# Performance work log

Hardware: AMD Instinct MI355X
Metric: run time of the kernel (lower is better)

## Reference

```python
import jax, jax.numpy as jnp
import numpy as np

N_SEQ, N_TOK, C_M, C, C_Z = 512, 384, 64, 32, 128


def setup_inputs() -> dict:
    key = jax.random.key(0)
    k1, k2, k3, k4 = jax.random.split(key, 4)
    scale = 1.0 / np.sqrt(C_M)
    return {
        "msa_feat": jax.random.normal(k1, (N_SEQ, N_TOK, C_M), dtype=jnp.float32),
        "msa_mask": jnp.ones((N_SEQ, N_TOK), dtype=jnp.float32),
        "gamma": jnp.ones((C_M,), dtype=jnp.float32),
        "beta": jnp.zeros((C_M,), dtype=jnp.float32),
        "Wa": jax.random.normal(k2, (C_M, C), dtype=jnp.float32) * scale,
        "Wb": jax.random.normal(k3, (C_M, C), dtype=jnp.float32) * scale,
        "Wout": jax.random.normal(k4, (C * C, C_Z), dtype=jnp.float32) * (1.0 / C),
        "bout": jnp.zeros((C_Z,), dtype=jnp.float32),
    }


def reference(msa_feat, msa_mask, gamma, beta, Wa, Wb, Wout, bout):
    # LayerNorm over c_m (eps matches torch default 1e-5)
    mu = jnp.mean(msa_feat, axis=-1, keepdims=True)
    var = jnp.mean(jnp.square(msa_feat - mu), axis=-1, keepdims=True)
    m = (msa_feat - mu) * jax.lax.rsqrt(var + 1e-5) * gamma + beta

    mask = msa_mask[..., None]                       # [s, i, 1]
    a = (m @ Wa) * mask                              # [s, i, c]
    b = (m @ Wb) * mask                              # [s, j, c]

    # Outer product contracted over MSA rows s: [i, j, c, c]
    ab = jnp.einsum('sic,sjd->ijcd', a, b)
    n_tok = a.shape[-2]
    ab = ab.reshape(n_tok, n_tok, C * C)             # [i, j, c*c]

    z = ab @ Wout + bout                             # [i, j, c_z]
    norm = jnp.einsum('si,sj->ij', msa_mask, msa_mask)
    return z / (norm[..., None] + 0.001)
```

## Files before the change

### kernel.cpp

```cpp
#include <hip/hip_runtime.h>
#include <cstdint>
#include <cstddef>

#define NS 512
#define NT 384
#define CZ 128

typedef __bf16 bf16x8 __attribute__((ext_vector_type(8)));
typedef __bf16 bf16x4 __attribute__((ext_vector_type(4)));
typedef float floatx16 __attribute__((ext_vector_type(16)));
typedef float floatx4 __attribute__((ext_vector_type(4)));


__global__ __launch_bounds__(256) void prep_wout(const float* __restrict__ Wout,
                                                 __bf16* __restrict__ WT) {
  const int idx = blockIdx.x * 256 + threadIdx.x;
  const int e = idx >> 10, kk = idx & 1023;
  const int round = kk >> 9, rem = kk & 511, d = rem >> 4, cp = rem & 15;
  const int c = round * 16 + cp;
  WT[idx] = (__bf16)Wout[(size_t)(c * 32 + d) * CZ + e];
}

__global__ __launch_bounds__(256) void prep_norm(const float* __restrict__ mask,
                                                 float* __restrict__ rnorm) {
  __shared__ float mi[512];
  const int i = blockIdx.x, t = threadIdx.x;
  mi[t]       = mask[(size_t)t * NT + i];
  mi[t + 256] = mask[(size_t)(t + 256) * NT + i];
  __syncthreads();
  for (int j = t; j < NT; j += 256) {
    float acc = 0.f;
#pragma unroll 4
    for (int s = 0; s < NS; ++s) acc += mi[s] * mask[(size_t)s * NT + j];
    rnorm[(size_t)i * NT + j] = 1.0f / (acc + 0.001f);
  }
}

__global__ __launch_bounds__(64) void ln_proj(const float* __restrict__ feat,
                                              const float* __restrict__ mask,
                                              const float* __restrict__ gamma,
                                              const float* __restrict__ beta,
                                              const float* __restrict__ Wa,
                                              const float* __restrict__ Wb,
                                              __bf16* __restrict__ Abf,
                                              __bf16* __restrict__ Bbf) {
  __shared__ __align__(16) __bf16 T[32 * 72];
  const int bid = blockIdx.x;
  const int i = bid >> 3;
  const int s0 = (bid & 7) << 6;
  const int lane = threadIdx.x;
  const int l31 = lane & 31, lh = lane >> 5;

  const float* frow = feat + ((size_t)(s0 + lane) * NT + i) * 64;
  float x[64];
#pragma unroll
  for (int q = 0; q < 16; ++q) {
    const float4 v = *(const float4*)(frow + q * 4);
    x[q * 4 + 0] = v.x; x[q * 4 + 1] = v.y;
    x[q * 4 + 2] = v.z; x[q * 4 + 3] = v.w;
  }

  float mu = 0.f;
#pragma unroll
  for (int k = 0; k < 64; ++k) mu += x[k];
  mu *= (1.0f / 64.0f);
  float var = 0.f;
#pragma unroll
  for (int k = 0; k < 64; ++k) { const float d = x[k] - mu; var += d * d; }
  var *= (1.0f / 64.0f);
  const float rstd = rsqrtf(var + 1e-5f);
#pragma unroll
  for (int k = 0; k < 64; ++k)
    x[k] = (x[k] - mu) * rstd * gamma[k] + beta[k];

  const float mv = mask[(size_t)(s0 + lane) * NT + i];

  float acc[32];
#pragma unroll
  for (int c = 0; c < 32; ++c) acc[c] = 0.f;
#pragma unroll 8
  for (int k = 0; k < 64; ++k) {
    const float mk = x[k];
#pragma unroll
    for (int c = 0; c < 32; ++c) acc[c] = fmaf(mk, Wa[k * 32 + c], acc[c]);
  }
#pragma unroll
  for (int c = 0; c < 32; ++c) T[c * 72 + lane] = (__bf16)(acc[c] * mv);
  __syncthreads();
  {
    __bf16* dst = Abf + (size_t)(i >> 2) * 65536 + (size_t)(s0 >> 3) * 1024 +
                  (size_t)((i & 3) * 32) * 8;
#pragma unroll
    for (int q = 0; q < 4; ++q) {
      const bf16x8 v = *(const bf16x8*)(T + l31 * 72 + (q * 2 + lh) * 8);
      *(bf16x8*)(dst + (size_t)(q * 2 + lh) * 1024 + l31 * 8) = v;
    }
  }
  __syncthreads();

#pragma unroll
  for (int c = 0; c < 32; ++c) acc[c] = 0.f;
#pragma unroll 8
  for (int k = 0; k < 64; ++k) {
    const float mk = x[k];
#pragma unroll
    for (int c = 0; c < 32; ++c) acc[c] = fmaf(mk, Wb[k * 32 + c], acc[c]);
  }
#pragma unroll
  for (int c = 0; c < 32; ++c) T[c * 72 + lane] = (__bf16)(acc[c] * mv);
  __syncthreads();
  {
    __bf16* dst = Bbf + (size_t)(i >> 3) * 131072 + (size_t)(s0 >> 3) * 2048 +
                  (size_t)((i & 7) * 32) * 8;
#pragma unroll
    for (int q = 0; q < 4; ++q) {
      const bf16x8 v = *(const bf16x8*)(T + l31 * 72 + (q * 2 + lh) * 8);
      *(bf16x8*)(dst + (size_t)(q * 2 + lh) * 2048 + l31 * 8) = v;
    }
  }
}

__global__ __launch_bounds__(512, 4) void opm_gemm(const __bf16* __restrict__ A,
                                                   const __bf16* __restrict__ B,
                                                   const __bf16* __restrict__ WT,
                                                   const float* __restrict__ bout,
                                                   const float* __restrict__ rnorm,
                                                   float* __restrict__ out) {
  __shared__ __align__(16) __bf16 smem[24576];

  const int tid = threadIdx.x, lane = tid & 63, wid = tid >> 6;
  const int wm = wid & 1, wn = wid >> 1;
  const int l31 = lane & 31, lh = lane >> 5;
  const int l15 = lane & 15, lq = lane >> 4;
  const int bm = blockIdx.x % 96, bn = blockIdx.x / 96;

  const __bf16* Apan = A + (size_t)bm * 65536;
  const __bf16* Bpan = B + (size_t)bn * 131072;

  floatx16 acc[2][2];
#pragma unroll
  for (int fm = 0; fm < 2; ++fm)
#pragma unroll
    for (int fn = 0; fn < 2; ++fn)
#pragma unroll
      for (int q = 0; q < 16; ++q) acc[fm][fn][q] = 0.f;

#define STAGE(kt, OFF)                                                          \
  {                                                                             \
    __bf16* dst = smem + (OFF);                                                 \
    __builtin_amdgcn_global_load_lds(                                           \
        (const __attribute__((address_space(1))) void*)(Apan +                  \
            (size_t)(kt) * 4096 + wid * 512 + lane * 8),                        \
        (__attribute__((address_space(3))) void*)(dst + wid * 512), 16, 0, 0);  \
    _Pragma("unroll")                                                           \
    for (int q = 0; q < 2; ++q) {                                               \
      const int g = q * 8 + wid;                                                \
      __builtin_amdgcn_global_load_lds(                                         \
          (const __attribute__((address_space(1))) void*)(Bpan +                \
              (size_t)(kt) * 8192 + g * 512 + lane * 8),                        \
          (__attribute__((address_space(3))) void*)(dst + 4096 + g * 512),      \
          16, 0, 0);                                                            \
    }                                                                           \
  }

  STAGE(0, 0);
  int buf = 0;
  for (int kt = 0; kt < 16; ++kt) {
    __syncthreads();
    if (kt < 15) STAGE(kt + 1, (buf ^ 1) * 12288);
    const __bf16* As = smem + buf * 12288;
    const __bf16* Bs = As + 4096;
    __builtin_amdgcn_s_setprio(1);
#pragma unroll
    for (int ks = 0; ks < 2; ++ks) {
      const int ck = ks * 2 + lh;
      bf16x8 af[2], bfv[2];
#pragma unroll
      for (int fm = 0; fm < 2; ++fm)
        af[fm] = *(const bf16x8*)(As + ck * 1024 + (wm * 64 + fm * 32 + l31) * 8);
#pragma unroll
      for (int fn = 0; fn < 2; ++fn)
        bfv[fn] = *(const bf16x8*)(Bs + ck * 2048 + (wn * 64 + fn * 32 + l31) * 8);
#pragma unroll
      for (int fm = 0; fm < 2; ++fm)
#pragma unroll
        for (int fn = 0; fn < 2; ++fn)
          acc[fm][fn] = __builtin_amdgcn_mfma_f32_32x32x16_bf16(af[fm], bfv[fn],
                                                                acc[fm][fn], 0, 0, 0);
    }
    __builtin_amdgcn_s_setprio(0);
    buf ^= 1;
  }
#undef STAGE

  floatx4 zf[2];
#pragma unroll
  for (int ps = 0; ps < 2; ++ps)
#pragma unroll
    for (int q = 0; q < 4; ++q) zf[ps][q] = 0.f;
  const int e0 = wid * 16;

#pragma unroll
  for (int round = 0; round < 2; ++round) {
    __syncthreads();
#pragma unroll
    for (int fm = 0; fm < 2; ++fm)
#pragma unroll
      for (int fn = 0; fn < 2; ++fn) {
        const int p = (wm * 2 + fm) * 8 + wn * 2 + fn;
        __bf16* base = smem + p * 648 + l31 * 20 + lh * 4;
#pragma unroll
        for (int qp = 0; qp < 2; ++qp) {
          bf16x4 v;
#pragma unroll
          for (int j = 0; j < 4; ++j)
            v[j] = (__bf16)acc[fm][fn][round * 8 + qp * 4 + j];
          *(bf16x4*)(base + qp * 8) = v;
        }
      }
    __syncthreads();
    const int pAddr = (lq >> 1) * 20 + (lq & 1) * 8;
    const __bf16* p0 = smem + l15 * 648 + pAddr;
    const __bf16* p1 = p0 + 16 * 648;
    const __bf16* w0 = WT + (size_t)(e0 + l15) * 1024 + round * 512 + lq * 8;
#pragma unroll 4
    for (int ks = 0; ks < 16; ++ks) {
      const bf16x8 pa0 = *(const bf16x8*)(p0 + ks * 40);
      const bf16x8 pa1 = *(const bf16x8*)(p1 + ks * 40);
      const bf16x8 wb = *(const bf16x8*)(w0 + ks * 32);
      zf[0] = __builtin_amdgcn_mfma_f32_16x16x32_bf16(pa0, wb, zf[0], 0, 0, 0);
      zf[1] = __builtin_amdgcn_mfma_f32_16x16x32_bf16(pa1, wb, zf[1], 0, 0, 0);
    }
  }

  {
    const int e = e0 + l15;
    const float be = bout[e];
#pragma unroll
    for (int ps = 0; ps < 2; ++ps)
#pragma unroll
      for (int q = 0; q < 4; ++q) {
        const int p = ps * 16 + lq * 4 + q;
        const int i = bm * 4 + (p >> 3), j = bn * 8 + (p & 7);
        const float rn = rnorm[(size_t)i * NT + j];
        out[((size_t)i * NT + j) * CZ + e] = (zf[ps][q] + be) * rn;
      }
  }
}

extern "C" void kernel_launch(void* const* d_in, const int* in_sizes, int n_in,
                              void* d_out, int out_size, void* d_ws, size_t ws_size,
                              hipStream_t stream) {
  const float* feat  = (const float*)d_in[0];
  const float* mask  = (const float*)d_in[1];
  const float* gamma = (const float*)d_in[2];
  const float* beta  = (const float*)d_in[3];
  const float* Wa    = (const float*)d_in[4];
  const float* Wb    = (const float*)d_in[5];
  const float* Wout  = (const float*)d_in[6];
  const float* bout  = (const float*)d_in[7];
  float* out = (float*)d_out;

  char* ws = (char*)d_ws;
  const size_t AB_BYTES = (size_t)96 * 65536 * sizeof(__bf16);
  __bf16* Abf = (__bf16*)(ws);
  __bf16* Bbf = (__bf16*)(ws + AB_BYTES);
  __bf16* WT  = (__bf16*)(ws + 2 * AB_BYTES);
  float* rnorm = (float*)(ws + 2 * AB_BYTES + (size_t)CZ * 1024 * sizeof(__bf16));

  prep_wout<<<512, 256, 0, stream>>>(Wout, WT);
  prep_norm<<<NT, 256, 0, stream>>>(mask, rnorm);
  ln_proj<<<NT * (NS / 64), 64, 0, stream>>>(feat, mask, gamma, beta, Wa, Wb, Abf, Bbf);
  opm_gemm<<<96 * 48, 512, 0, stream>>>(Abf, Bbf, WT, bout, rnorm, out);
}
```

Baseline: 425.0 us.

## Compute mask normalization with bf16 MFMA after transposing mask

Replaces the scalar per-row mask outer-product kernel with two kernels: one transposes the mask into bf16 in scratch space (reusing the Abf region before ln_proj overwrites it), and one computes the i×j mask-count matrix with 32x32x16 bf16 MFMA tiles. This is meant to cut the cost of the O(NT²·NS) scalar loop in prep_norm. Bf16 holds 0/1 mask values exactly, but fractional masks would lose precision. It adds a launch.

```diff
diff --git a/kernel.cpp b/kernel.cpp
--- a/kernel.cpp
+++ b/kernel.cpp
@@ -21,18 +21,49 @@
   WT[idx] = (__bf16)Wout[(size_t)(c * 32 + d) * CZ + e];
 }
 
-__global__ __launch_bounds__(256) void prep_norm(const float* __restrict__ mask,
+__global__ __launch_bounds__(256) void prep_maskT(const float* __restrict__ mask,
+                                                  __bf16* __restrict__ MT) {
+  __shared__ __bf16 TT[64 * 72];
+  const int s0 = (blockIdx.x & 7) * 64, j0 = (blockIdx.x >> 3) * 64;
+  const int t = threadIdx.x;
+  const int row = t >> 4, col0 = (t & 15) * 4;
+#pragma unroll
+  for (int rr = 0; rr < 4; ++rr) {
+    const int r = rr * 16 + row;
+    const float4 v = *(const float4*)(mask + (size_t)(s0 + r) * NT + j0 + col0);
+    TT[(col0 + 0) * 72 + r] = (__bf16)v.x;
+    TT[(col0 + 1) * 72 + r] = (__bf16)v.y;
+    TT[(col0 + 2) * 72 + r] = (__bf16)v.z;
+    TT[(col0 + 3) * 72 + r] = (__bf16)v.w;
+  }
+  __syncthreads();
+#pragma unroll
+  for (int h = 0; h < 2; ++h) {
+    const int jr = h * 32 + (t >> 3), sc = (t & 7) * 8;
+    *(bf16x8*)(MT + (size_t)(j0 + jr) * 512 + s0 + sc) =
+        *(const bf16x8*)(TT + jr * 72 + sc);
+  }
+}
+
+__global__ __launch_bounds__(64) void prep_norm2(const __bf16* __restrict__ MT,
                                                  float* __restrict__ rnorm) {
-  __shared__ float mi[512];
-  const int i = blockIdx.x, t = threadIdx.x;
-  mi[t]       = mask[(size_t)t * NT + i];
-  mi[t + 256] = mask[(size_t)(t + 256) * NT + i];
-  __syncthreads();
-  for (int j = t; j < NT; j += 256) {
-    float acc = 0.f;
-#pragma unroll 4
-    for (int s = 0; s < NS; ++s) acc += mi[s] * mask[(size_t)s * NT + j];
-    rnorm[(size_t)i * NT + j] = 1.0f / (acc + 0.001f);
+  const int i0 = (blockIdx.x % 12) * 32, j0 = (blockIdx.x / 12) * 32;
+  const int lane = threadIdx.x, l31 = lane & 31, lh = lane >> 5;
+  floatx16 acc;
+#pragma unroll
+  for (int q = 0; q < 16; ++q) acc[q] = 0.f;
+  const __bf16* arow = MT + (size_t)(i0 + l31) * 512 + lh * 8;
+  const __bf16* brow = MT + (size_t)(j0 + l31) * 512 + lh * 8;
+#pragma unroll 8
+  for (int kc = 0; kc < 32; ++kc) {
+    const bf16x8 a = *(const bf16x8*)(arow + kc * 16);
+    const bf16x8 b = *(const bf16x8*)(brow + kc * 16);
+    acc = __builtin_amdgcn_mfma_f32_32x32x16_bf16(a, b, acc, 0, 0, 0);
+  }
+#pragma unroll
+  for (int r = 0; r < 16; ++r) {
+    const int il = (r & 3) + 4 * lh + 8 * (r >> 2);
+    rnorm[(size_t)(i0 + il) * NT + j0 + l31] = 1.0f / (acc[r] + 0.001f);
   }
 }
 
@@ -267,9 +298,11 @@
   __bf16* Bbf = (__bf16*)(ws + AB_BYTES);
   __bf16* WT  = (__bf16*)(ws + 2 * AB_BYTES);
   float* rnorm = (float*)(ws + 2 * AB_BYTES + (size_t)CZ * 1024 * sizeof(__bf16));
+  __bf16* MT = (__bf16*)(ws);
 
   prep_wout<<<512, 256, 0, stream>>>(Wout, WT);
-  prep_norm<<<NT, 256, 0, stream>>>(mask, rnorm);
+  prep_maskT<<<48, 256, 0, stream>>>(mask, MT);
+  prep_norm2<<<144, 64, 0, stream>>>(MT, rnorm);
   ln_proj<<<NT * (NS / 64), 64, 0, stream>>>(feat, mask, gamma, beta, Wa, Wb, Abf, Bbf);
   opm_gemm<<<96 * 48, 512, 0, stream>>>(Abf, Bbf, WT, bout, rnorm, out);
 }
```

New measurement: 378.1 us. 11.0% less time.
